# Optimization experiments

Measured on AMD Instinct MI355X. Metric: run time of the kernel, lower is better.

Reference implementation:

```python
import jax, jax.numpy as jnp
import numpy as np

B, S, H = 2, 1024, 4096
NH, NKV, HD = 32, 8, 128
GROUPS = NH // NKV  # 4


def _dequant_linear(x, w_q, scale, bias=None):
    # torch Linear layout: W [out, in]; per-output-channel symmetric dequant
    w = w_q.astype(jnp.float32) * scale[:, None]
    y = jnp.einsum('bsi,oi->bso', x, w)
    if bias is not None:
        y = y + bias
    return y


def setup_inputs() -> dict:
    key = jax.random.key(0)
    ks = jax.random.split(key, 12)
    hidden_states = jax.random.normal(ks[0], (B, S, H), dtype=jnp.float32)
    # additive causal mask: 0 on/below diagonal, large negative above
    causal = jnp.where(jnp.tril(jnp.ones((S, S), dtype=bool)), 0.0, -1e9).astype(jnp.float32)
    attention_mask = jnp.broadcast_to(causal[None, None], (B, 1, S, S))
    # int8-valued quantized weights, per-out-channel scales (~unit-variance effective weight rows / sqrt(fan_in))
    def qw(k, out, inp):
        return jax.random.randint(k, (out, inp), -127, 128, dtype=jnp.int32)
    def sc(k, out):
        return jax.random.uniform(k, (out,), dtype=jnp.float32, minval=1e-4, maxval=3e-4)
    wq_q = qw(ks[1], H, H);            wq_s = sc(ks[2], H)
    wk_q = qw(ks[3], NKV * HD, H);     wk_s = sc(ks[4], NKV * HD)
    wv_q = qw(ks[5], NKV * HD, H);     wv_s = sc(ks[6], NKV * HD)
    wo_q = qw(ks[7], H, H);            wo_s = sc(ks[8], H)
    bq = jax.random.normal(ks[9], (H,), dtype=jnp.float32) * 0.02
    bk = jax.random.normal(ks[10], (NKV * HD,), dtype=jnp.float32) * 0.02
    return {
        'hidden_states': hidden_states, 'attention_mask': attention_mask,
        'wq_q': wq_q, 'wq_s': wq_s, 'bq': bq,
        'wk_q': wk_q, 'wk_s': wk_s, 'bk': bk,
        'wv_q': wv_q, 'wv_s': wv_s,
        'wo_q': wo_q, 'wo_s': wo_s,
    }


def reference(hidden_states, attention_mask, wq_q, wq_s, bq, wk_q, wk_s, bk, wv_q, wv_s, wo_q, wo_s):
    bsz, q_len, _ = hidden_states.shape
    q = _dequant_linear(hidden_states, wq_q, wq_s, bq)      # [B,S,H]
    k = _dequant_linear(hidden_states, wk_q, wk_s, bk)      # [B,S,NKV*HD]
    v = _dequant_linear(hidden_states, wv_q, wv_s)          # [B,S,NKV*HD]
    q = q.reshape(bsz, q_len, NH, HD).transpose(0, 2, 1, 3)     # [B,NH,S,HD]
    k = k.reshape(bsz, q_len, NKV, HD).transpose(0, 2, 1, 3)    # [B,NKV,S,HD]
    v = v.reshape(bsz, q_len, NKV, HD).transpose(0, 2, 1, 3)
    # GQA: repeat_interleave kv heads along head dim
    k = jnp.repeat(k, GROUPS, axis=1)   # [B,NH,S,HD]
    v = jnp.repeat(v, GROUPS, axis=1)
    scores = jnp.einsum('bhqd,bhkd->bhqk', q, k) / np.float32(np.sqrt(HD))
    scores = scores + attention_mask
    attn = jax.nn.softmax(scores.astype(jnp.float32), axis=-1).astype(q.dtype)
    out = jnp.einsum('bhqk,bhkd->bhqd', attn, v)            # [B,NH,S,HD]
    out = out.transpose(0, 2, 1, 3).reshape(bsz, q_len, H)
    out = _dequant_linear(out, wo_q, wo_s)
    return out
```

## Files before the change

### kernel.cpp

```cpp
#include <hip/hip_runtime.h>
#include <math.h>

#define BB   2
#define SS   1024
#define HH   4096
#define NHH  32
#define NKVV 8
#define HDD  128
#define MR   2048
#define KVD  1024
#define NQKVD 6144
#define KD   4096
#define KHALF 2048
#define SCALE2_F 0.12751744f

typedef __attribute__((ext_vector_type(8))) short bf16x8;
typedef __attribute__((ext_vector_type(4))) float f32x4;
typedef __attribute__((ext_vector_type(4))) int i32x4;

#define MFMA(a, b, c) __builtin_amdgcn_mfma_f32_16x16x32_bf16((a), (b), (c), 0, 0, 0)
#define MFMA_I8(a, b, c) __builtin_amdgcn_mfma_i32_16x16x64_i8((a), (b), (c), 0, 0, 0)

__device__ __forceinline__ unsigned short f2bf(float f) {
  union { float f; unsigned u; } v; v.f = f;
  return (unsigned short)((v.u + 0x7fffu + ((v.u >> 16) & 1u)) >> 16);
}
__device__ __forceinline__ unsigned short f2h(float f) {
  union { _Float16 h; unsigned short s; } v; v.h = (_Float16)f; return v.s;
}
__device__ __forceinline__ float h2f(unsigned short s) {
  union { unsigned short s; _Float16 h; } v; v.s = s; return (float)v.h;
}
__device__ __forceinline__ float bf2f(unsigned short s) {
  union { unsigned u; float f; } v; v.u = ((unsigned)s) << 16; return v.f;
}
__device__ __forceinline__ float4 ld4h(const unsigned short* p) {
  uint2 d = *(const uint2*)p;
  float4 r;
  r.x = h2f((unsigned short)(d.x & 0xffff)); r.y = h2f((unsigned short)(d.x >> 16));
  r.z = h2f((unsigned short)(d.y & 0xffff)); r.w = h2f((unsigned short)(d.y >> 16));
  return r;
}
__device__ __forceinline__ float exp2_fast(float x) {
  float r; asm("v_exp_f32 %0, %1" : "=v"(r) : "v"(x)); return r;
}
__device__ __forceinline__ unsigned cvt_pk_bf16(float a, float b) {
  unsigned r; asm("v_cvt_pk_bf16_f32 %0, %1, %2" : "=v"(r) : "v"(a), "v"(b)); return r;
}

__device__ __forceinline__ void gload_lds16(const void* g, void* l) {
  __builtin_amdgcn_global_load_lds(
      (const __attribute__((address_space(1))) void*)g,
      (__attribute__((address_space(3))) void*)l, 16, 0, 0);
}

__device__ __forceinline__ signed char q8(float x, float inv) {
  float r = rintf(x * inv);
  r = fmaxf(-127.f, fminf(127.f, r));
  return (signed char)(int)r;
}

#define NQ16 ((size_t)HH * HH / 16)
#define NK16 ((size_t)KVD * HH / 16)
__global__ void cvt_w_all(const int* __restrict__ wq, const int* __restrict__ wk,
                          const int* __restrict__ wv, const int* __restrict__ wo,
                          signed char* __restrict__ wqkv, signed char* __restrict__ wo8) {
  size_t i = (size_t)blockIdx.x * 256 + threadIdx.x;
  const int* src;
  signed char* dst;
  if (i < NQ16) { src = wq; dst = wqkv; }
  else if (i < NQ16 + NK16) { src = wk - NQ16 * 16; dst = wqkv; }
  else if (i < NQ16 + 2 * NK16) { src = wv - (NQ16 + NK16) * 16; dst = wqkv; }
  else { src = wo - (NQ16 + 2 * NK16) * 16; dst = wo8 - (NQ16 + 2 * NK16) * 16; }
  const int4* p = (const int4*)(src + i * 16);
  union { signed char c[16]; int4 q; } o;
#pragma unroll
  for (int j = 0; j < 4; ++j) {
    int4 v = p[j];
    o.c[j * 4 + 0] = (signed char)v.x; o.c[j * 4 + 1] = (signed char)v.y;
    o.c[j * 4 + 2] = (signed char)v.z; o.c[j * 4 + 3] = (signed char)v.w;
  }
  *(int4*)(dst + i * 16) = o.q;
}

__global__ void quant_f32(const float* __restrict__ in, signed char* __restrict__ out,
                          float* __restrict__ scale) {
  __shared__ float wm[4];
  const int row = blockIdx.x;
  const int t = threadIdx.x;
  const float4* p = (const float4*)(in + (size_t)row * HH) + t * 4;
  float4 v[4];
  float m = 0.f;
#pragma unroll
  for (int j = 0; j < 4; ++j) {
    v[j] = p[j];
    m = fmaxf(m, fmaxf(fmaxf(fabsf(v[j].x), fabsf(v[j].y)), fmaxf(fabsf(v[j].z), fabsf(v[j].w))));
  }
#pragma unroll
  for (int o = 32; o; o >>= 1) m = fmaxf(m, __shfl_xor(m, o));
  if ((t & 63) == 0) wm[t >> 6] = m;
  __syncthreads();
  m = fmaxf(fmaxf(wm[0], wm[1]), fmaxf(wm[2], wm[3]));
  m = fmaxf(m, 1e-12f);
  const float inv = 127.f / m;
  union { signed char c[16]; int4 q; } o;
#pragma unroll
  for (int j = 0; j < 4; ++j) {
    o.c[j * 4 + 0] = q8(v[j].x, inv); o.c[j * 4 + 1] = q8(v[j].y, inv);
    o.c[j * 4 + 2] = q8(v[j].z, inv); o.c[j * 4 + 3] = q8(v[j].w, inv);
  }
  ((int4*)(out + (size_t)row * HH))[t] = o.q;
  if (t == 0) scale[row] = m / 127.f;
}

__global__ void quant_bf16(const unsigned short* __restrict__ in, signed char* __restrict__ out,
                           float* __restrict__ scale) {
  __shared__ float wm[4];
  const int row = blockIdx.x;
  const int t = threadIdx.x;
  const uint4* p = (const uint4*)(in + (size_t)row * HH) + t * 2;
  float f[16];
  float m = 0.f;
#pragma unroll
  for (int j = 0; j < 2; ++j) {
    uint4 d = p[j];
    unsigned u[4] = {d.x, d.y, d.z, d.w};
#pragma unroll
    for (int k = 0; k < 4; ++k) {
      f[j * 8 + k * 2] = bf2f((unsigned short)(u[k] & 0xffff));
      f[j * 8 + k * 2 + 1] = bf2f((unsigned short)(u[k] >> 16));
    }
  }
#pragma unroll
  for (int e = 0; e < 16; ++e) m = fmaxf(m, fabsf(f[e]));
#pragma unroll
  for (int o = 32; o; o >>= 1) m = fmaxf(m, __shfl_xor(m, o));
  if ((t & 63) == 0) wm[t >> 6] = m;
  __syncthreads();
  m = fmaxf(fmaxf(wm[0], wm[1]), fmaxf(wm[2], wm[3]));
  m = fmaxf(m, 1e-12f);
  const float inv = 127.f / m;
  union { signed char c[16]; int4 q; } o;
#pragma unroll
  for (int e = 0; e < 16; ++e) o.c[e] = q8(f[e], inv);
  ((int4*)(out + (size_t)row * HH))[t] = o.q;
  if (t == 0) scale[row] = m / 127.f;
}

template <int MODE>
__global__ __launch_bounds__(256) void gemm_i8(
    const signed char* __restrict__ A, const signed char* __restrict__ W,
    const float* __restrict__ sRow,
    const float* __restrict__ s0, const float* __restrict__ s1, const float* __restrict__ s2,
    unsigned short* __restrict__ P, int N) {
  __shared__ signed char ldsA[128 * 128];
  __shared__ signed char ldsB[128 * 128];
  const int t = threadIdx.x;
  const int lane = t & 63;
  const int w = t >> 6;
  const int wr = w & 1, wc = w >> 1;
  const int l15 = lane & 15, quad = lane >> 4;
  const int bm = blockIdx.y, bn = blockIdx.x, kz = blockIdx.z;

  const int srow_ = t >> 3;
  const int scol_ = ((t & 7) ^ (srow_ & 7)) * 16;
  const signed char* gA = A + (size_t)(bm * 128 + srow_) * KD + scol_ + kz * KHALF;
  const signed char* gW = W + (size_t)(bn * 128 + srow_) * KD + scol_ + kz * KHALF;
  signed char* lA = ldsA + t * 16;
  signed char* lB = ldsB + t * 16;

  i32x4 acc[4][4] = {};

  for (int k0 = 0; k0 < KHALF; k0 += 128) {
    __syncthreads();
#pragma unroll
    for (int j = 0; j < 4; ++j) {
      gload_lds16(gA + (size_t)j * 32 * KD + k0, lA + j * 4096);
      gload_lds16(gW + (size_t)j * 32 * KD + k0, lB + j * 4096);
    }
    __syncthreads();
#pragma unroll
    for (int kc = 0; kc < 2; ++kc) {
      i32x4 af[4], bfr[4];
#pragma unroll
      for (int mi = 0; mi < 4; ++mi) {
        const int row = wr * 64 + mi * 16 + l15;
        const int ch = (kc * 4 + quad) ^ (row & 7);
        af[mi] = *(const i32x4*)(ldsA + row * 128 + ch * 16);
      }
#pragma unroll
      for (int ni = 0; ni < 4; ++ni) {
        const int row = wc * 64 + ni * 16 + l15;
        const int ch = (kc * 4 + quad) ^ (row & 7);
        bfr[ni] = *(const i32x4*)(ldsB + row * 128 + ch * 16);
      }
#pragma unroll
      for (int mi = 0; mi < 4; ++mi)
#pragma unroll
        for (int ni = 0; ni < 4; ++ni)
          acc[mi][ni] = MFMA_I8(af[mi], bfr[ni], acc[mi][ni]);
    }
  }

  unsigned short* Pz = P + (size_t)kz * MR * N;
  const int row0 = bm * 128 + wr * 64 + quad * 4;
  const int col0 = bn * 128 + wc * 64 + l15;
#pragma unroll
  for (int ni = 0; ni < 4; ++ni) {
    const int col = col0 + ni * 16;
    float sc;
    if (MODE == 0)
      sc = (col < HH) ? s0[col] : (col < HH + KVD) ? s1[col - HH] : s2[col - HH - KVD];
    else
      sc = s0[col];
#pragma unroll
    for (int mi = 0; mi < 4; ++mi)
#pragma unroll
      for (int r = 0; r < 4; ++r) {
        const int row = row0 + mi * 16 + r;
        const float v = (float)acc[mi][ni][r] * sRow[row] * sc;
        Pz[(size_t)row * N + col] = f2h(v);
      }
  }
}

__global__ void epi_qkv(const unsigned short* __restrict__ P0, const unsigned short* __restrict__ P1,
                        const float* __restrict__ bQ, const float* __restrict__ bK,
                        unsigned short* __restrict__ oQ, unsigned short* __restrict__ oK,
                        unsigned short* __restrict__ oVt) {
  __shared__ unsigned short lds_t[64][65];
  const int t = threadIdx.x;
  int bid = blockIdx.x;
  if (bid < 10240) {
    const int row = bid / 5;
    const int col = (bid - row * 5) * 1024 + t * 4;
    const size_t off = (size_t)row * NQKVD + col;
    float4 a = ld4h(P0 + off), b2 = ld4h(P1 + off);
    union { unsigned short s[4]; uint2 d; } o;
    if (col < HH) {
      const float4 b = *(const float4*)(bQ + col);
      o.s[0] = f2bf((a.x + b2.x + b.x) * SCALE2_F);
      o.s[1] = f2bf((a.y + b2.y + b.y) * SCALE2_F);
      o.s[2] = f2bf((a.z + b2.z + b.z) * SCALE2_F);
      o.s[3] = f2bf((a.w + b2.w + b.w) * SCALE2_F);
      *(uint2*)(oQ + (size_t)row * HH + col) = o.d;
    } else {
      const int c = col - HH;
      const float4 b = *(const float4*)(bK + c);
      o.s[0] = f2bf(a.x + b2.x + b.x); o.s[1] = f2bf(a.y + b2.y + b.y);
      o.s[2] = f2bf(a.z + b2.z + b.z); o.s[3] = f2bf(a.w + b2.w + b.w);
      *(uint2*)(oK + (size_t)row * KVD + c) = o.d;
    }
  } else {
    bid -= 10240;
    const int c0 = (bid & 15) * 64;
    const int r0 = (bid >> 4) * 64;
    const int c4 = (t & 15) * 4;
#pragma unroll
    for (int rr = 0; rr < 4; ++rr) {
      const int rl = (t >> 4) * 4 + rr;
      const size_t off = (size_t)(r0 + rl) * NQKVD + (HH + KVD) + c0 + c4;
      float4 a = ld4h(P0 + off), b = ld4h(P1 + off);
      lds_t[c4 + 0][rl] = f2bf(a.x + b.x);
      lds_t[c4 + 1][rl] = f2bf(a.y + b.y);
      lds_t[c4 + 2][rl] = f2bf(a.z + b.z);
      lds_t[c4 + 3][rl] = f2bf(a.w + b.w);
    }
    __syncthreads();
    const int cl = t >> 2;
    const int rs = (t & 3) * 16;
    union { unsigned short s[16]; uint4 q[2]; } o;
#pragma unroll
    for (int i = 0; i < 16; ++i) o.s[i] = lds_t[cl][rs + i];
    uint4* dst = (uint4*)(oVt + (size_t)(c0 + cl) * MR + r0 + rs);
    dst[0] = o.q[0]; dst[1] = o.q[1];
  }
}

__global__ void epi_o(const unsigned short* __restrict__ P0, const unsigned short* __restrict__ P1,
                      float* __restrict__ out) {
  const int col = (blockIdx.x * 256 + threadIdx.x) * 4;
  const int row = blockIdx.y;
  const size_t off = (size_t)row * HH + col;
  float4 a = ld4h(P0 + off), b = ld4h(P1 + off);
  *(float4*)(out + off) = make_float4(a.x + b.x, a.y + b.y, a.z + b.z, a.w + b.w);
}

__global__ __launch_bounds__(256, 2) void attn_kernel(
    const unsigned short* __restrict__ Q,
    const unsigned short* __restrict__ K,
    const unsigned short* __restrict__ Vt,
    unsigned short* __restrict__ O) {
  __shared__ unsigned short ldsK[2][64][128];
  __shared__ unsigned short ldsV[2][2 * 128 * 32];
  __shared__ unsigned short ldsP[4][16 * 88];
  const int t = threadIdx.x;
  const int lane = t & 63;
  const int wv = t >> 6;
  const int l15 = lane & 15, quad = lane >> 4;
  const int qt = 15 - blockIdx.x;
  const int h = blockIdx.y;
  const int b = blockIdx.z;
  const int kv = h >> 2;
  const int q0w = qt * 64 + wv * 16;
  const int q = q0w + l15;

  bf16x8 bq[4];
  const unsigned short* qbase = Q + (size_t)(b * SS + q0w + l15) * HH + h * HDD + quad * 8;
#pragma unroll
  for (int kk = 0; kk < 4; ++kk) bq[kk] = *(const bf16x8*)(qbase + kk * 32);

  const int srow = t >> 4;
  const int schunk = (t & 15) ^ (srow & 7);
  const unsigned short* gK = K + (size_t)(b * SS + srow) * KVD + kv * HDD + schunk * 8;
  const unsigned short* gV = Vt + (size_t)(kv * HDD + wv * 32 + (lane >> 2)) * MR + b * SS + (lane & 3) * 8;
  unsigned short* lV = &ldsV[0][0] + wv * 1024 + lane * 8;
  unsigned short* lp = ldsP[wv];

  f32x4 accO[8] = {};
  float m_run = -1e30f, l_part = 0.f;

#pragma unroll
  for (int j = 0; j < 4; ++j)
    gload_lds16(gK + (size_t)j * 16 * KVD, &ldsK[0][j * 16][0] + t * 8);
#pragma unroll
  for (int kc = 0; kc < 2; ++kc)
#pragma unroll
    for (int j = 0; j < 2; ++j)
      gload_lds16(gV + (size_t)j * 16 * MR + kc * 32, lV + kc * 4096 + j * 512);
  __syncthreads();

  int cur = 0;
  for (int kt = 0; kt <= qt; ++kt) {
    const int k0 = kt * 64;
    if (kt < qt) {
#pragma unroll
      for (int j = 0; j < 4; ++j)
        gload_lds16(gK + (size_t)(k0 + 64 + j * 16) * KVD,
                    &ldsK[cur ^ 1][j * 16][0] + t * 8);
#pragma unroll
      for (int kc = 0; kc < 2; ++kc)
#pragma unroll
        for (int j = 0; j < 2; ++j)
          gload_lds16(gV + (size_t)j * 16 * MR + k0 + 64 + kc * 32,
                      lV + (cur ^ 1) * 8192 + kc * 4096 + j * 512);
    }

    f32x4 st[4] = {};
    __builtin_amdgcn_s_setprio(1);
#pragma unroll
    for (int kk = 0; kk < 4; ++kk)
#pragma unroll
      for (int mf = 0; mf < 4; ++mf) {
        const int r = mf * 16 + l15;
        bf16x8 af = *(const bf16x8*)(&ldsK[cur][r][((kk * 4 + quad) ^ (r & 7)) * 8]);
        st[mf] = MFMA(af, bq[kk], st[mf]);
      }
    __builtin_amdgcn_s_setprio(0);

    float p[4][4];
#pragma unroll
    for (int mf = 0; mf < 4; ++mf)
#pragma unroll
      for (int r = 0; r < 4; ++r) p[mf][r] = st[mf][r];
    if (kt == qt) {
#pragma unroll
      for (int mf = 0; mf < 4; ++mf)
#pragma unroll
        for (int r = 0; r < 4; ++r) {
          const int k = k0 + mf * 16 + quad * 4 + r;
          if (k > q) p[mf][r] = -1e30f;
        }
    }
    float cm = -1e30f;
#pragma unroll
    for (int mf = 0; mf < 4; ++mf)
#pragma unroll
      for (int r = 0; r < 4; ++r) cm = fmaxf(cm, p[mf][r]);
    cm = fmaxf(cm, __shfl_xor(cm, 16));
    cm = fmaxf(cm, __shfl_xor(cm, 32));

    if (!__all(cm <= m_run + 8.f)) {
      const float mn = fmaxf(m_run, cm);
      const float al = exp2_fast(m_run - mn);
      l_part *= al;
      m_run = mn;
      float af4[4];
#pragma unroll
      for (int r = 0; r < 4; ++r) af4[r] = __shfl(al, quad * 4 + r);
#pragma unroll
      for (int cb = 0; cb < 8; ++cb)
#pragma unroll
        for (int r = 0; r < 4; ++r) accO[cb][r] *= af4[r];
    }

#pragma unroll
    for (int mf = 0; mf < 4; ++mf) {
      const float e0 = exp2_fast(p[mf][0] - m_run);
      const float e1 = exp2_fast(p[mf][1] - m_run);
      const float e2 = exp2_fast(p[mf][2] - m_run);
      const float e3 = exp2_fast(p[mf][3] - m_run);
      l_part += (e0 + e1) + (e2 + e3);
      union { unsigned u[2]; unsigned long long d; } pk;
      pk.u[0] = cvt_pk_bf16(e0, e1);
      pk.u[1] = cvt_pk_bf16(e2, e3);
      *(unsigned long long*)(lp + l15 * 88 + mf * 16 + quad * 4) = pk.d;
    }
    bf16x8 ap0 = *(const bf16x8*)(lp + l15 * 88 + quad * 8);
    bf16x8 ap1 = *(const bf16x8*)(lp + l15 * 88 + 32 + quad * 8);

    __builtin_amdgcn_s_setprio(1);
#pragma unroll
    for (int cb = 0; cb < 8; ++cb) {
      bf16x8 bv0 = *(const bf16x8*)(&ldsV[cur][0] + (cb * 16 + l15) * 32 + quad * 8);
      bf16x8 bv1 = *(const bf16x8*)(&ldsV[cur][0] + 4096 + (cb * 16 + l15) * 32 + quad * 8);
      accO[cb] = MFMA(ap0, bv0, accO[cb]);
      accO[cb] = MFMA(ap1, bv1, accO[cb]);
    }
    __builtin_amdgcn_s_setprio(0);

    __syncthreads();
    cur ^= 1;
  }

  l_part += __shfl_xor(l_part, 16);
  l_part += __shfl_xor(l_part, 32);
  float lr[4];
#pragma unroll
  for (int r = 0; r < 4; ++r) lr[r] = __shfl(l_part, quad * 4 + r);
  unsigned short* ob = O + (size_t)(b * SS + q0w + quad * 4) * HH + h * HDD + l15;
#pragma unroll
  for (int cb = 0; cb < 8; ++cb)
#pragma unroll
    for (int r = 0; r < 4; ++r)
      ob[(size_t)r * HH + cb * 16] = f2bf(accO[cb][r] / lr[r]);
}

extern "C" void kernel_launch(void* const* d_in, const int* in_sizes, int n_in,
                              void* d_out, int out_size, void* d_ws, size_t ws_size,
                              hipStream_t stream) {
  const float* x = (const float*)d_in[0];
  const int* wq = (const int*)d_in[2];
  const float* wqs = (const float*)d_in[3];
  const float* bq = (const float*)d_in[4];
  const int* wk = (const int*)d_in[5];
  const float* wks = (const float*)d_in[6];
  const float* bk = (const float*)d_in[7];
  const int* wv = (const int*)d_in[8];
  const float* wvs = (const float*)d_in[9];
  const int* wo = (const int*)d_in[10];
  const float* wos = (const float*)d_in[11];
  float* out = (float*)d_out;
  char* ws = (char*)d_ws;

  signed char*    x_i8    = (signed char*)   (ws + (0ull   << 20));
  signed char*    wqkv_i8 = (signed char*)   (ws + (8ull   << 20));
  signed char*    wo_i8   = (signed char*)   (ws + (32ull  << 20));
  unsigned short* Pq      = (unsigned short*)(ws + (48ull  << 20));
  unsigned short* q_bf    = (unsigned short*)(ws + (0ull   << 20));
  unsigned short* k_bf    = (unsigned short*)(ws + (16ull  << 20));
  unsigned short* v_t     = (unsigned short*)(ws + (20ull  << 20));
  unsigned short* a_bf    = (unsigned short*)(ws + (48ull  << 20));
  signed char*    a_i8    = (signed char*)   (ws + (64ull  << 20));
  unsigned short* Po      = (unsigned short*)(ws + (96ull  << 20));
  float*          sx      = (float*)         (ws + (128ull << 20));
  float*          sa      = (float*)         (ws + (129ull << 20));
  if (ws_size < (130ull << 20)) return;

  quant_f32<<<MR, 256, 0, stream>>>(x, x_i8, sx);
  cvt_w_all<<<10240, 256, 0, stream>>>(wq, wk, wv, wo, wqkv_i8, wo_i8);

  gemm_i8<0><<<dim3(NQKVD / 128, MR / 128, 2), 256, 0, stream>>>(
      x_i8, wqkv_i8, sx, wqs, wks, wvs, Pq, NQKVD);

  epi_qkv<<<10752, 256, 0, stream>>>(Pq, Pq + (size_t)MR * NQKVD, bq, bk, q_bf, k_bf, v_t);

  attn_kernel<<<dim3(16, NHH, BB), 256, 0, stream>>>(q_bf, k_bf, v_t, a_bf);

  quant_bf16<<<MR, 256, 0, stream>>>(a_bf, a_i8, sa);
  gemm_i8<1><<<dim3(HH / 128, MR / 128, 2), 256, 0, stream>>>(
      a_i8, wo_i8, sa, wos, nullptr, nullptr, Po, HH);
  epi_o<<<dim3(4, MR), 256, 0, stream>>>(Po, Po + (size_t)MR * HH, out);
}
```

Measured before the change: 424.8 us.

## Drop split-K and fuse QKV and output epilogues into int8 GEMM

The int8 GEMMs now run over the full K dimension instead of two halves. Dequant, bias, Q scaling, bf16 conversion and the V transpose are written directly from the accumulators, and the output projection writes fp32 straight to the output. This removes the fp16 partial buffers, their round trip through memory, and the separate epi_qkv and epi_o kernels. In exchange the grids are halved and each block runs a longer K loop, which reduces parallelism.

```diff
diff --git a/kernel.cpp b/kernel.cpp
--- a/kernel.cpp
+++ b/kernel.cpp
@@ -11,7 +11,6 @@
 #define KVD  1024
 #define NQKVD 6144
 #define KD   4096
-#define KHALF 2048
 #define SCALE2_F 0.12751744f
 
 typedef __attribute__((ext_vector_type(8))) short bf16x8;
@@ -25,21 +24,8 @@
   union { float f; unsigned u; } v; v.f = f;
   return (unsigned short)((v.u + 0x7fffu + ((v.u >> 16) & 1u)) >> 16);
 }
-__device__ __forceinline__ unsigned short f2h(float f) {
-  union { _Float16 h; unsigned short s; } v; v.h = (_Float16)f; return v.s;
-}
-__device__ __forceinline__ float h2f(unsigned short s) {
-  union { unsigned short s; _Float16 h; } v; v.s = s; return (float)v.h;
-}
 __device__ __forceinline__ float bf2f(unsigned short s) {
   union { unsigned u; float f; } v; v.u = ((unsigned)s) << 16; return v.f;
-}
-__device__ __forceinline__ float4 ld4h(const unsigned short* p) {
-  uint2 d = *(const uint2*)p;
-  float4 r;
-  r.x = h2f((unsigned short)(d.x & 0xffff)); r.y = h2f((unsigned short)(d.x >> 16));
-  r.z = h2f((unsigned short)(d.y & 0xffff)); r.w = h2f((unsigned short)(d.y >> 16));
-  return r;
 }
 __device__ __forceinline__ float exp2_fast(float x) {
   float r; asm("v_exp_f32 %0, %1" : "=v"(r) : "v"(x)); return r;
@@ -152,7 +138,9 @@
     const signed char* __restrict__ A, const signed char* __restrict__ W,
     const float* __restrict__ sRow,
     const float* __restrict__ s0, const float* __restrict__ s1, const float* __restrict__ s2,
-    unsigned short* __restrict__ P, int N) {
+    const float* __restrict__ bQ, const float* __restrict__ bK,
+    unsigned short* __restrict__ oQ, unsigned short* __restrict__ oK,
+    unsigned short* __restrict__ oVt, float* __restrict__ oF) {
   __shared__ signed char ldsA[128 * 128];
   __shared__ signed char ldsB[128 * 128];
   const int t = threadIdx.x;
@@ -160,18 +148,18 @@
   const int w = t >> 6;
   const int wr = w & 1, wc = w >> 1;
   const int l15 = lane & 15, quad = lane >> 4;
-  const int bm = blockIdx.y, bn = blockIdx.x, kz = blockIdx.z;
+  const int bm = blockIdx.y, bn = blockIdx.x;
 
   const int srow_ = t >> 3;
   const int scol_ = ((t & 7) ^ (srow_ & 7)) * 16;
-  const signed char* gA = A + (size_t)(bm * 128 + srow_) * KD + scol_ + kz * KHALF;
-  const signed char* gW = W + (size_t)(bn * 128 + srow_) * KD + scol_ + kz * KHALF;
+  const signed char* gA = A + (size_t)(bm * 128 + srow_) * KD + scol_;
+  const signed char* gW = W + (size_t)(bn * 128 + srow_) * KD + scol_;
   signed char* lA = ldsA + t * 16;
   signed char* lB = ldsB + t * 16;
 
   i32x4 acc[4][4] = {};
 
-  for (int k0 = 0; k0 < KHALF; k0 += 128) {
+  for (int k0 = 0; k0 < KD; k0 += 128) {
     __syncthreads();
 #pragma unroll
     for (int j = 0; j < 4; ++j) {
@@ -202,88 +190,68 @@
     }
   }
 
-  unsigned short* Pz = P + (size_t)kz * MR * N;
   const int row0 = bm * 128 + wr * 64 + quad * 4;
   const int col0 = bn * 128 + wc * 64 + l15;
-#pragma unroll
-  for (int ni = 0; ni < 4; ++ni) {
-    const int col = col0 + ni * 16;
-    float sc;
-    if (MODE == 0)
-      sc = (col < HH) ? s0[col] : (col < HH + KVD) ? s1[col - HH] : s2[col - HH - KVD];
-    else
-      sc = s0[col];
-#pragma unroll
-    for (int mi = 0; mi < 4; ++mi)
-#pragma unroll
-      for (int r = 0; r < 4; ++r) {
-        const int row = row0 + mi * 16 + r;
-        const float v = (float)acc[mi][ni][r] * sRow[row] * sc;
-        Pz[(size_t)row * N + col] = f2h(v);
+  if (MODE == 1) {
+#pragma unroll
+    for (int ni = 0; ni < 4; ++ni) {
+      const int col = col0 + ni * 16;
+      const float sc = s0[col];
+#pragma unroll
+      for (int mi = 0; mi < 4; ++mi)
+#pragma unroll
+        for (int r = 0; r < 4; ++r) {
+          const int row = row0 + mi * 16 + r;
+          oF[(size_t)row * HH + col] = (float)acc[mi][ni][r] * sRow[row] * sc;
+        }
+    }
+  } else if (col0 < HH) {
+#pragma unroll
+    for (int ni = 0; ni < 4; ++ni) {
+      const int col = col0 + ni * 16;
+      const float sc = s0[col];
+      const float bv = bQ[col];
+#pragma unroll
+      for (int mi = 0; mi < 4; ++mi)
+#pragma unroll
+        for (int r = 0; r < 4; ++r) {
+          const int row = row0 + mi * 16 + r;
+          oQ[(size_t)row * HH + col] =
+              f2bf(((float)acc[mi][ni][r] * sRow[row] * sc + bv) * SCALE2_F);
+        }
+    }
+  } else if (col0 < HH + KVD) {
+#pragma unroll
+    for (int ni = 0; ni < 4; ++ni) {
+      const int col = col0 + ni * 16;
+      const float sc = s1[col - HH];
+      const float bv = bK[col - HH];
+#pragma unroll
+      for (int mi = 0; mi < 4; ++mi)
+#pragma unroll
+        for (int r = 0; r < 4; ++r) {
+          const int row = row0 + mi * 16 + r;
+          oK[(size_t)row * KVD + (col - HH)] =
+              f2bf((float)acc[mi][ni][r] * sRow[row] * sc + bv);
+        }
+    }
+  } else {
+#pragma unroll
+    for (int ni = 0; ni < 4; ++ni) {
+      const int c = col0 + ni * 16 - (HH + KVD);
+      const float sc = s2[c];
+#pragma unroll
+      for (int mi = 0; mi < 4; ++mi) {
+        union { unsigned short s[4]; unsigned long long d; } pk;
+#pragma unroll
+        for (int r = 0; r < 4; ++r) {
+          const int row = row0 + mi * 16 + r;
+          pk.s[r] = f2bf((float)acc[mi][ni][r] * sRow[row] * sc);
+        }
+        *(unsigned long long*)(oVt + (size_t)c * MR + row0 + mi * 16) = pk.d;
       }
-  }
-}
-
-__global__ void epi_qkv(const unsigned short* __restrict__ P0, const unsigned short* __restrict__ P1,
-                        const float* __restrict__ bQ, const float* __restrict__ bK,
-                        unsigned short* __restrict__ oQ, unsigned short* __restrict__ oK,
-                        unsigned short* __restrict__ oVt) {
-  __shared__ unsigned short lds_t[64][65];
-  const int t = threadIdx.x;
-  int bid = blockIdx.x;
-  if (bid < 10240) {
-    const int row = bid / 5;
-    const int col = (bid - row * 5) * 1024 + t * 4;
-    const size_t off = (size_t)row * NQKVD + col;
-    float4 a = ld4h(P0 + off), b2 = ld4h(P1 + off);
-    union { unsigned short s[4]; uint2 d; } o;
-    if (col < HH) {
-      const float4 b = *(const float4*)(bQ + col);
-      o.s[0] = f2bf((a.x + b2.x + b.x) * SCALE2_F);
-      o.s[1] = f2bf((a.y + b2.y + b.y) * SCALE2_F);
-      o.s[2] = f2bf((a.z + b2.z + b.z) * SCALE2_F);
-      o.s[3] = f2bf((a.w + b2.w + b.w) * SCALE2_F);
-      *(uint2*)(oQ + (size_t)row * HH + col) = o.d;
-    } else {
-      const int c = col - HH;
-      const float4 b = *(const float4*)(bK + c);
-      o.s[0] = f2bf(a.x + b2.x + b.x); o.s[1] = f2bf(a.y + b2.y + b.y);
-      o.s[2] = f2bf(a.z + b2.z + b.z); o.s[3] = f2bf(a.w + b2.w + b.w);
-      *(uint2*)(oK + (size_t)row * KVD + c) = o.d;
-    }
-  } else {
-    bid -= 10240;
-    const int c0 = (bid & 15) * 64;
-    const int r0 = (bid >> 4) * 64;
-    const int c4 = (t & 15) * 4;
-#pragma unroll
-    for (int rr = 0; rr < 4; ++rr) {
-      const int rl = (t >> 4) * 4 + rr;
-      const size_t off = (size_t)(r0 + rl) * NQKVD + (HH + KVD) + c0 + c4;
-      float4 a = ld4h(P0 + off), b = ld4h(P1 + off);
-      lds_t[c4 + 0][rl] = f2bf(a.x + b.x);
-      lds_t[c4 + 1][rl] = f2bf(a.y + b.y);
-      lds_t[c4 + 2][rl] = f2bf(a.z + b.z);
-      lds_t[c4 + 3][rl] = f2bf(a.w + b.w);
-    }
-    __syncthreads();
-    const int cl = t >> 2;
-    const int rs = (t & 3) * 16;
-    union { unsigned short s[16]; uint4 q[2]; } o;
-#pragma unroll
-    for (int i = 0; i < 16; ++i) o.s[i] = lds_t[cl][rs + i];
-    uint4* dst = (uint4*)(oVt + (size_t)(c0 + cl) * MR + r0 + rs);
-    dst[0] = o.q[0]; dst[1] = o.q[1];
-  }
-}
-
-__global__ void epi_o(const unsigned short* __restrict__ P0, const unsigned short* __restrict__ P1,
-                      float* __restrict__ out) {
-  const int col = (blockIdx.x * 256 + threadIdx.x) * 4;
-  const int row = blockIdx.y;
-  const size_t off = (size_t)row * HH + col;
-  float4 a = ld4h(P0 + off), b = ld4h(P1 + off);
-  *(float4*)(out + off) = make_float4(a.x + b.x, a.y + b.y, a.z + b.z, a.w + b.w);
+    }
+  }
 }
 
 __global__ __launch_bounds__(256, 2) void attn_kernel(
@@ -456,13 +424,11 @@
   signed char*    x_i8    = (signed char*)   (ws + (0ull   << 20));
   signed char*    wqkv_i8 = (signed char*)   (ws + (8ull   << 20));
   signed char*    wo_i8   = (signed char*)   (ws + (32ull  << 20));
-  unsigned short* Pq      = (unsigned short*)(ws + (48ull  << 20));
-  unsigned short* q_bf    = (unsigned short*)(ws + (0ull   << 20));
-  unsigned short* k_bf    = (unsigned short*)(ws + (16ull  << 20));
-  unsigned short* v_t     = (unsigned short*)(ws + (20ull  << 20));
-  unsigned short* a_bf    = (unsigned short*)(ws + (48ull  << 20));
-  signed char*    a_i8    = (signed char*)   (ws + (64ull  << 20));
-  unsigned short* Po      = (unsigned short*)(ws + (96ull  << 20));
+  unsigned short* q_bf    = (unsigned short*)(ws + (48ull  << 20));
+  unsigned short* k_bf    = (unsigned short*)(ws + (64ull  << 20));
+  unsigned short* v_t     = (unsigned short*)(ws + (68ull  << 20));
+  unsigned short* a_bf    = (unsigned short*)(ws + (72ull  << 20));
+  signed char*    a_i8    = (signed char*)   (ws + (88ull  << 20));
   float*          sx      = (float*)         (ws + (128ull << 20));
   float*          sa      = (float*)         (ws + (129ull << 20));
   if (ws_size < (130ull << 20)) return;
@@ -470,15 +436,14 @@
   quant_f32<<<MR, 256, 0, stream>>>(x, x_i8, sx);
   cvt_w_all<<<10240, 256, 0, stream>>>(wq, wk, wv, wo, wqkv_i8, wo_i8);
 
-  gemm_i8<0><<<dim3(NQKVD / 128, MR / 128, 2), 256, 0, stream>>>(
-      x_i8, wqkv_i8, sx, wqs, wks, wvs, Pq, NQKVD);
-
-  epi_qkv<<<10752, 256, 0, stream>>>(Pq, Pq + (size_t)MR * NQKVD, bq, bk, q_bf, k_bf, v_t);
+  gemm_i8<0><<<dim3(NQKVD / 128, MR / 128), 256, 0, stream>>>(
+      x_i8, wqkv_i8, sx, wqs, wks, wvs, bq, bk, q_bf, k_bf, v_t, nullptr);
 
   attn_kernel<<<dim3(16, NHH, BB), 256, 0, stream>>>(q_bf, k_bf, v_t, a_bf);
 
   quant_bf16<<<MR, 256, 0, stream>>>(a_bf, a_i8, sa);
-  gemm_i8<1><<<dim3(HH / 128, MR / 128, 2), 256, 0, stream>>>(
-      a_i8, wo_i8, sa, wos, nullptr, nullptr, Po, HH);
-  epi_o<<<dim3(4, MR), 256, 0, stream>>>(Po, Po + (size_t)MR * HH, out);
-}
+
+  gemm_i8<1><<<dim3(HH / 128, MR / 128), 256, 0, stream>>>(
+      a_i8, wo_i8, sa, wos, nullptr, nullptr, nullptr, nullptr,
+      nullptr, nullptr, nullptr, out);
+}
```

Measured after the change: 398.8 us. 6.1% less time.
